# Kernel tuning notes

Measured on AMD Instinct MI355X. Metric: run time of the kernel, lower is better.

The kernel has to match this reference:

```python
import jax, jax.numpy as jnp
import numpy as np

DG = 8            # deformable_groups
MAX_RES = 10.0    # max_residual_magnitude
K = 9             # 3x3 kernel positions


def conv3(x, w, b):
    y = jax.lax.conv_general_dilated(x, w, (1, 1), [(1, 1), (1, 1)],
                                     dimension_numbers=('NCHW', 'OIHW', 'NCHW'))
    return y + b[None, :, None, None]


def lrelu(v):
    return jnp.where(v >= 0, v, 0.1 * v)


def deform_conv2d(x, offset, mask, weight, bias):
    # x: [B,C,H,W]; offset: [B,2*DG*K,H,W] (per group, K points, (y,x) interleaved)
    # mask: [B,DG*K,H,W]; weight: [O,C,3,3]; stride=1, pad=1, dil=1, groups=1
    B, C, H, W = x.shape
    Cg = C // DG
    off = offset.reshape(B, DG, K, 2, H, W)
    dtype = x.dtype
    dy = (jnp.arange(K) // 3 - 1).astype(dtype)
    dx = (jnp.arange(K) % 3 - 1).astype(dtype)
    py = off[:, :, :, 0] + jnp.arange(H, dtype=dtype)[None, None, None, :, None] + dy[None, None, :, None, None]
    px = off[:, :, :, 1] + jnp.arange(W, dtype=dtype)[None, None, None, None, :] + dx[None, None, :, None, None]
    y0 = jnp.floor(py)
    x0 = jnp.floor(px)
    x_flat = x.reshape(B, DG, Cg, H * W)
    m = mask.reshape(B, DG, K, H, W)
    acc = jnp.zeros((B, DG, Cg, K, H, W), dtype=dtype)
    for iy, wy in ((y0, y0 + 1.0 - py), (y0 + 1.0, py - y0)):
        for ix, wx in ((x0, x0 + 1.0 - px), (x0 + 1.0, px - x0)):
            valid = (iy >= 0) & (iy < H) & (ix >= 0) & (ix < W)
            yi = jnp.clip(iy, 0, H - 1).astype(jnp.int32)
            xi = jnp.clip(ix, 0, W - 1).astype(jnp.int32)
            idx = (yi * W + xi).reshape(B, DG, 1, K * H * W)
            g = jnp.take_along_axis(x_flat, idx, axis=3).reshape(B, DG, Cg, K, H, W)
            wgt = (wy * wx * valid.astype(dtype) * m)[:, :, None]  # mask folded in
            acc = acc + g * wgt
    O = weight.shape[0]
    out = jnp.einsum('bgckhw,ogck->bohw', acc, weight.reshape(O, DG, Cg, K))
    return out + bias[None, :, None, None]


def setup_inputs() -> dict:
    key = jax.random.key(0)
    ks = jax.random.split(key, 12)
    B, C, H, W = 4, 64, 128, 128
    inp = {
        'x': jax.random.normal(ks[0], (B, C, H, W), jnp.float32),
        'x_warped0': jax.random.normal(ks[1], (B, C, H, W), jnp.float32),
        'x_current': jax.random.normal(ks[2], (B, C, H, W), jnp.float32),
        'flow0': jax.random.normal(ks[3], (B, 2, H, W), jnp.float32),
        'w1': jax.random.normal(ks[4], (64, 130, 3, 3), jnp.float32) * 0.05,
        'b1': jnp.zeros((64,), jnp.float32),
        'w2': jax.random.normal(ks[5], (64, 64, 3, 3), jnp.float32) * 0.05,
        'b2': jnp.zeros((64,), jnp.float32),
        'w3': jax.random.normal(ks[6], (64, 64, 3, 3), jnp.float32) * 0.05,
        'b3': jnp.zeros((64,), jnp.float32),
        'w4': jax.random.normal(ks[7], (216, 64, 3, 3), jnp.float32) * 0.05,
        'b4': jnp.zeros((216,), jnp.float32),
        'weight': jax.random.normal(ks[8], (64, 64, 3, 3), jnp.float32) * 0.05,
        'bias': jnp.zeros((64,), jnp.float32),
    }
    return inp


def reference(x, x_warped0, x_current, flow0, w1, b1, w2, b2, w3, b3, w4, b4, weight, bias):
    # conv_offset stack on cat([x_warped0, x_current, flow0])
    feat = jnp.concatenate([x_warped0, x_current, flow0], axis=1)  # [B, 2C+2, H, W]
    o = lrelu(conv3(feat, w1, b1))
    o = lrelu(conv3(o, w2, b2))
    o = lrelu(conv3(o, w3, b3))
    o = conv3(o, w4, b4)  # [B, 3*K*DG, H, W]
    out1, out2, mask = jnp.split(o, 3, axis=1)
    offset = MAX_RES * jnp.tanh(jnp.concatenate([out1, out2], axis=1))  # [B, 2*K*DG, H, W]
    # flows[0].flip(1).repeat(1, K*DG, 1, 1): (y,x) flow tiled over all sample points
    offset = offset + jnp.tile(flow0[:, ::-1], (1, K * DG, 1, 1))
    mask = jax.nn.sigmoid(mask)
    return deform_conv2d(x, offset, mask, weight, bias)
```

## Files before the change

kernel.cpp:

```cpp
#include <hip/hip_runtime.h>
#include <math.h>

#define HH 128
#define WW 128
#define BB 4
#define HW (HH*WW)

typedef unsigned short u16;
typedef unsigned int u32;
typedef __bf16 bf16x8 __attribute__((ext_vector_type(8)));
typedef float f32x4 __attribute__((ext_vector_type(4)));

__device__ __forceinline__ u16 f2bf(float x) {
    u32 u = __float_as_uint(x);
    return (u16)((u + 0x7fffu + ((u >> 16) & 1u)) >> 16);
}
__device__ __forceinline__ float bf2f(u16 h) {
    return __uint_as_float(((u32)h) << 16);
}
__device__ __forceinline__ bf16x8 ld8(const u16* p) {
    union { uint4 u; bf16x8 v; } c;
    c.u = *(const uint4*)p;
    return c.v;
}
__device__ __forceinline__ bf16x8 cvt8(uint4 u) {
    union { uint4 u; bf16x8 v; } c;
    c.u = u;
    return c.v;
}

__global__ void split_w_k(const float* __restrict__ src, u16* __restrict__ dh,
                          u16* __restrict__ dl, int OC, int OCpad, int CIN, int CINpad)
{
    const int i = blockIdx.x * 256 + threadIdx.x;
    const int tot = OCpad * 9 * CINpad;
    if (i >= tot) return;
    const int oc = i / (9 * CINpad);
    const int r = i - oc * 9 * CINpad;
    const int tap = r / CINpad;
    const int cin = r - tap * CINpad;
    float v = 0.f;
    if (oc < OC && cin < CIN) v = src[((size_t)oc * CIN + cin) * 9 + tap];
    const u16 h = f2bf(v);
    dh[i] = h;
    dl[i] = f2bf(v - bf2f(h));
}

__global__ void pad_bias_k(const float* __restrict__ b, float* __restrict__ bp)
{
    const int i = blockIdx.x * 256 + threadIdx.x;
    if (i < 256) bp[i] = (i < 216) ? b[i] : 0.f;
}

__global__ void pack_dw_k(const float* __restrict__ wt, u16* __restrict__ Apack)
{
    const int i = blockIdx.x * 256 + threadIdx.x;
    if (i >= 36864) return;
    const int jj = i & 7;
    const int fr = (i >> 3) & 15;
    const int m  = (i >> 7) & 3;
    const int fq = (i >> 9) & 3;
    const int kk = i >> 11;
    const int oc = m * 16 + fr;
    const int j  = kk * 32 + fq * 8 + jj;
    const int tap = j >> 3, c = j & 7;
    const int g = tap / 9, kt = tap - g * 9;
    const int ch = g * 8 + c;
    Apack[i] = f2bf(wt[((size_t)oc * 64 + ch) * 9 + kt]);
}

template<int CREC>
__global__ __launch_bounds__(256) void pack_x_k(
    const float* __restrict__ A, const float* __restrict__ B2,
    const float* __restrict__ C3, u16* __restrict__ dst)
{
    const int i = blockIdx.x * 256 + threadIdx.x;
    const int b = i >> 14;
    const int px = i & 16383;
    u16* rec = dst + (size_t)i * (CREC * 2);

#pragma unroll
    for (int g = 0; g < CREC / 32; ++g) {
#pragma unroll
        for (int cb = 0; cb < 4; ++cb) {
            u32 hwv[4], lwv[4];
#pragma unroll
            for (int p = 0; p < 4; ++p) {
                float v[2];
#pragma unroll
                for (int e = 0; e < 2; ++e) {
                    const int c = g * 32 + cb * 8 + p * 2 + e;
                    float vv;
                    if (c < 64)       vv = A[((size_t)(b * 64 + c)) * HW + px];
                    else if (c < 128) vv = B2[((size_t)(b * 64 + c - 64)) * HW + px];
                    else if (c < 130) vv = C3[((size_t)(b * 2 + c - 128)) * HW + px];
                    else              vv = 0.f;
                    v[e] = vv;
                }
                const u16 h0 = f2bf(v[0]), h1 = f2bf(v[1]);
                const u16 l0 = f2bf(v[0] - bf2f(h0)), l1 = f2bf(v[1] - bf2f(h1));
                hwv[p] = (u32)h0 | ((u32)h1 << 16);
                lwv[p] = (u32)l0 | ((u32)l1 << 16);
            }
            uint4 H; H.x = hwv[0]; H.y = hwv[1]; H.z = hwv[2]; H.w = hwv[3];
            uint4 L; L.x = lwv[0]; L.y = lwv[1]; L.z = lwv[2]; L.w = lwv[3];
            *(uint4*)(rec + g * 64 + cb * 16)     = H;
            *(uint4*)(rec + g * 64 + cb * 16 + 8) = L;
        }
    }
}

template<int NCHUNK, int KGLAST, int MODE, bool RELU, bool PACKOUT, int MINW>
__global__ __launch_bounds__(256, MINW) void conv_pk_k(
    const u16* __restrict__ Xp, const u16* __restrict__ Wh, const u16* __restrict__ Wl,
    const float* __restrict__ bias, float* __restrict__ outf, u16* __restrict__ outp,
    int OCreal)
{
    const int ROWS = (MODE == 1) ? 8 : 4;
    const int NPX = (ROWS + 2) * 18;
    __shared__ u16 Xs[NPX * 136];
    const int CINpad = (NCHUNK - 1) * 64 + KGLAST * 32;
    const int CRECU16 = CINpad * 2;

    const int tile = blockIdx.x;
    const int h0 = (tile >> 3) * ROWS;
    const int w0 = (tile & 7) * 16;
    const int b = blockIdx.z;
    const int t = threadIdx.x;
    const int lane = t & 63, wv = t >> 6;
    const int fr = lane & 15, fq = lane >> 4;

    const int mg = wv >> 1, rg = wv & 1;
    const int mbase = (MODE == 1) ? (blockIdx.y * 8 + mg * 4) : 0;

    f32x4 acc0[4];
    f32x4 acc1[4][4];
    if (MODE == 0) {
        const float4 bv = *(const float4*)(bias + wv * 16 + 4 * fq);
#pragma unroll
        for (int n = 0; n < 4; ++n) {
            acc0[n][0] = bv.x; acc0[n][1] = bv.y; acc0[n][2] = bv.z; acc0[n][3] = bv.w;
        }
    } else {
#pragma unroll
        for (int m = 0; m < 4; ++m) {
            const float4 bv = *(const float4*)(bias + (mbase + m) * 16 + 4 * fq);
#pragma unroll
            for (int n = 0; n < 4; ++n) {
                acc1[m][n][0] = bv.x; acc1[m][n][1] = bv.y;
                acc1[m][n][2] = bv.z; acc1[m][n][3] = bv.w;
            }
        }
    }

    const u16* WhL = Wh + (size_t)fr * 9 * CINpad + 8 * fq;
    const u16* WlL = Wl + (size_t)fr * 9 * CINpad + 8 * fq;

#pragma unroll
    for (int chunk = 0; chunk < NCHUNK; ++chunk) {
        const int nkg = (chunk == NCHUNK - 1) ? KGLAST : 2;
        const int nu = nkg * 8;
        __syncthreads();
        for (int s = t; s < NPX * nu; s += 256) {
            const int px = s / nu, o = s - px * nu;
            const int hy = px / 18, hx = px - hy * 18;
            const int gy = h0 + hy - 1, gx = w0 + hx - 1;
            uint4 v; v.x = 0; v.y = 0; v.z = 0; v.w = 0;
            if (gy >= 0 && gy < HH && gx >= 0 && gx < WW)
                v = *(const uint4*)(Xp + ((size_t)(b * HW + gy * WW + gx)) * CRECU16
                                       + chunk * 128 + o * 8);
            *(uint4*)(Xs + px * 136 + o * 8) = v;
        }
        __syncthreads();

        if (MODE == 0) {
#pragma unroll
            for (int tap = 0; tap < 9; ++tap) {
                const int ky = tap / 3, kx = tap % 3;
#pragma unroll
                for (int kg = 0; kg < 2; ++kg) {
                    if (kg >= nkg) break;
                    const size_t off = (size_t)(wv * 144 + tap) * CINpad + chunk * 64 + kg * 32;
                    const bf16x8 Ah = ld8(WhL + off);
                    const bf16x8 Al = ld8(WlL + off);
#pragma unroll
                    for (int n = 0; n < 4; ++n) {
                        const int hp = (n + ky) * 18 + fr + kx;
                        const u16* Bp = Xs + hp * 136 + kg * 64 + fq * 16;
                        const bf16x8 Bh = ld8(Bp);
                        const bf16x8 Bl = ld8(Bp + 8);
                        acc0[n] = __builtin_amdgcn_mfma_f32_16x16x32_bf16(Ah, Bh, acc0[n], 0, 0, 0);
                        acc0[n] = __builtin_amdgcn_mfma_f32_16x16x32_bf16(Ah, Bl, acc0[n], 0, 0, 0);
                        acc0[n] = __builtin_amdgcn_mfma_f32_16x16x32_bf16(Al, Bh, acc0[n], 0, 0, 0);
                    }
                }
            }
        } else {
            auto PF = [&](int tap, bf16x8 (&Dh)[8], bf16x8 (&Dl)[8]) {
#pragma unroll
                for (int kg = 0; kg < 2; ++kg)
#pragma unroll
                    for (int m = 0; m < 4; ++m) {
                        const size_t off = (size_t)((mbase + m) * 144 + tap) * CINpad
                                         + chunk * 64 + kg * 32;
                        Dh[kg * 4 + m] = ld8(WhL + off);
                        Dl[kg * 4 + m] = ld8(WlL + off);
                    }
            };
            auto CMP = [&](int tap, bf16x8 (&Dh)[8], bf16x8 (&Dl)[8]) {
                const int ky = tap / 3, kx = tap - 3 * ky;
#pragma unroll
                for (int kg = 0; kg < 2; ++kg) {
#pragma unroll
                    for (int n = 0; n < 4; ++n) {
                        const int hp = (rg * 4 + n + ky) * 18 + fr + kx;
                        const u16* Bp = Xs + hp * 136 + kg * 64 + fq * 16;
                        const bf16x8 Bh = ld8(Bp);
                        const bf16x8 Bl = ld8(Bp + 8);
#pragma unroll
                        for (int m = 0; m < 4; ++m) {
                            acc1[m][n] = __builtin_amdgcn_mfma_f32_16x16x32_bf16(Dh[kg * 4 + m], Bh, acc1[m][n], 0, 0, 0);
                            acc1[m][n] = __builtin_amdgcn_mfma_f32_16x16x32_bf16(Dh[kg * 4 + m], Bl, acc1[m][n], 0, 0, 0);
                            acc1[m][n] = __builtin_amdgcn_mfma_f32_16x16x32_bf16(Dl[kg * 4 + m], Bh, acc1[m][n], 0, 0, 0);
                        }
                    }
                }
            };

            bf16x8 PaH[8], PaL[8], PbH[8], PbL[8];
            PF(0, PaH, PaL);
#pragma unroll 1
            for (int tp = 0; tp < 4; ++tp) {
                PF(2 * tp + 1, PbH, PbL);
                CMP(2 * tp, PaH, PaL);
                PF(2 * tp + 2, PaH, PaL);
                CMP(2 * tp + 1, PbH, PbL);
            }
            CMP(8, PaH, PaL);
        }
    }

    if (MODE == 1) {
#pragma unroll
        for (int m = 0; m < 4; ++m)
#pragma unroll
            for (int n = 0; n < 4; ++n)
#pragma unroll
                for (int i = 0; i < 4; ++i) {
                    const int oc = (mbase + m) * 16 + 4 * fq + i;
                    if (oc < OCreal) {
                        float v = acc1[m][n][i];
                        if (RELU) v = (v >= 0.f) ? v : 0.1f * v;
                        outf[((size_t)(b * OCreal + oc)) * HW + (h0 + rg * 4 + n) * WW + w0 + fr] = v;
                    }
                }
    } else if (!PACKOUT) {
#pragma unroll
        for (int n = 0; n < 4; ++n)
#pragma unroll
            for (int i = 0; i < 4; ++i) {
                const int oc = wv * 16 + 4 * fq + i;
                if (oc < OCreal) {
                    float v = acc0[n][i];
                    if (RELU) v = (v >= 0.f) ? v : 0.1f * v;
                    outf[((size_t)(b * OCreal + oc)) * HW + (h0 + n) * WW + w0 + fr] = v;
                }
            }
    } else {
        __syncthreads();
        const int coff = (wv >> 1) * 64 + (((wv << 1) + (fq >> 1)) & 3) * 16 + ((fq & 1) << 2);
#pragma unroll
        for (int n = 0; n < 4; ++n) {
            u16 hh[4], ll[4];
#pragma unroll
            for (int i = 0; i < 4; ++i) {
                float v = acc0[n][i];
                if (RELU) v = (v >= 0.f) ? v : 0.1f * v;
                hh[i] = f2bf(v);
                ll[i] = f2bf(v - bf2f(hh[i]));
            }
            uint2 H, L;
            H.x = (u32)hh[0] | ((u32)hh[1] << 16);
            H.y = (u32)hh[2] | ((u32)hh[3] << 16);
            L.x = (u32)ll[0] | ((u32)ll[1] << 16);
            L.y = (u32)ll[2] | ((u32)ll[3] << 16);
            const int pxe = n * 16 + fr;
            u16* E = Xs + pxe * 136 + coff;
            *(uint2*)E = H;
            *(uint2*)(E + 8) = L;
        }
        __syncthreads();
        for (int i = t; i < 1024; i += 256) {
            const int px = i >> 4, o = i & 15;
            const uint4 v = *(const uint4*)(Xs + px * 136 + o * 8);
            const int gp = (h0 + (px >> 4)) * WW + w0 + (px & 15);
            *(uint4*)(outp + ((size_t)(b * HW + gp)) * 128 + o * 8) = v;
        }
    }
}

__global__ __launch_bounds__(256) void transpose_xq_k(
    const float* __restrict__ x, float4* __restrict__ xq)
{
    const int i = blockIdx.x * 256 + threadIdx.x;
    const int pix = i & (HW - 1);
    const int q = (i >> 14) & 15;
    const int b = i >> 18;
    const float* xp = x + ((size_t)(b * 64 + q * 4)) * HW + pix;
    float4 v;
    v.x = xp[0]; v.y = xp[HW]; v.z = xp[2 * HW]; v.w = xp[3 * HW];
    xq[(size_t)(b * 16 + q) * HW + pix] = v;
}

__device__ __forceinline__ unsigned pk_bf16(float lo, float hi) {
    unsigned a = __float_as_uint(lo), b = __float_as_uint(hi);
    return ((a + 0x8000u) >> 16) | ((b + 0x8000u) & 0xffff0000u);
}

__global__ __launch_bounds__(256, 4) void deform_fused_k(
    const float4* __restrict__ xq, const float* __restrict__ o4,
    const float* __restrict__ flow, const uint4* __restrict__ Apack,
    const float* __restrict__ bias, float* __restrict__ out)
{
    __shared__ u16 sv[32 * 584];

    const int bid = blockIdx.x;
    const int b = bid >> 9;
    const int pix0 = (bid & 511) << 5;
    const int t = threadIdx.x;

    {
        const int gpx = t & 31, g = t >> 5;
        const int pix = pix0 + gpx;
        const int h = pix >> 7, w = pix & (WW - 1);
        const float fy = flow[((size_t)b * 2 + 1) * HW + pix];
        const float fx = flow[((size_t)b * 2 + 0) * HW + pix];
        const float* ob = o4 + (size_t)b * 216 * HW + pix;
        const float4* q0 = xq + (size_t)(b * 16 + g * 2) * HW;
        const float4* q1 = q0 + HW;

        int   code[9];
        float w00[9], w01[9], w10[9], w11[9];

#pragma unroll
        for (int k = 0; k < 9; ++k) {
            const float oy = ob[(size_t)(g * 18 + k * 2) * HW];
            const float ox = ob[(size_t)(g * 18 + k * 2 + 1) * HW];
            float mm = ob[(size_t)(144 + g * 9 + k) * HW];
            mm = __builtin_amdgcn_rcpf(1.f + __expf(-mm));

            const float ay = fabsf(oy), ax = fabsf(ox);
            const float ey = __expf(-2.f * ay), ex = __expf(-2.f * ax);
            float ty = (1.f - ey) * __builtin_amdgcn_rcpf(1.f + ey);
            float tx = (1.f - ex) * __builtin_amdgcn_rcpf(1.f + ex);
            ty = copysignf(ty, oy); tx = copysignf(tx, ox);

            const float ppy = 10.f * ty + fy + (float)(h + k / 3 - 1);
            const float ppx = 10.f * tx + fx + (float)(w + k % 3 - 1);

            const float y0f = floorf(ppy), x0f = floorf(ppx);
            const float ly = ppy - y0f, lx = ppx - x0f;
            const int iy0 = (int)y0f, ix0 = (int)x0f;
            const int iy1 = iy0 + 1,  ix1 = ix0 + 1;

            const float vy0 = (iy0 >= 0 && iy0 < HH) ? 1.f : 0.f;
            const float vy1 = (iy1 >= 0 && iy1 < HH) ? 1.f : 0.f;
            const float vx0 = (ix0 >= 0 && ix0 < WW) ? 1.f : 0.f;
            const float vx1 = (ix1 >= 0 && ix1 < WW) ? 1.f : 0.f;

            const int cy0 = min(max(iy0, 0), HH - 1);
            const int cy1 = min(max(iy1, 0), HH - 1);
            const int cx0 = min(max(ix0, 0), WW - 1);
            const int cx1 = min(max(ix1, 0), WW - 1);

            w00[k] = (1.f - ly) * (1.f - lx) * vy0 * vx0 * mm;
            w01[k] = (1.f - ly) * lx         * vy0 * vx1 * mm;
            w10[k] = ly         * (1.f - lx) * vy1 * vx0 * mm;
            w11[k] = ly         * lx         * vy1 * vx1 * mm;

            code[k] = (cy0 * WW + cx0) | ((cx1 - cx0) << 14) | ((cy1 - cy0) << 15);
        }

        u16* svp = sv + gpx * 584 + g * 72;
#pragma unroll
        for (int k = 0; k < 9; ++k) {
            const int i00 = code[k] & 16383;
            const int i01 = i00 + ((code[k] >> 14) & 1);
            const int i10 = i00 + (((code[k] >> 15) & 1) << 7);
            const int i11 = i10 + ((code[k] >> 14) & 1);

            const float4 a0 = q0[i00], a1 = q1[i00];
            const float4 b0 = q0[i01], b1 = q1[i01];
            const float4 c0 = q0[i10], c1 = q1[i10];
            const float4 d0 = q0[i11], d1 = q1[i11];
            const float W00 = w00[k], W01 = w01[k], W10 = w10[k], W11 = w11[k];

            float s0 = W00 * a0.x + W01 * b0.x + W10 * c0.x + W11 * d0.x;
            float s1 = W00 * a0.y + W01 * b0.y + W10 * c0.y + W11 * d0.y;
            float s2 = W00 * a0.z + W01 * b0.z + W10 * c0.z + W11 * d0.z;
            float s3 = W00 * a0.w + W01 * b0.w + W10 * c0.w + W11 * d0.w;
            float s4 = W00 * a1.x + W01 * b1.x + W10 * c1.x + W11 * d1.x;
            float s5 = W00 * a1.y + W01 * b1.y + W10 * c1.y + W11 * d1.y;
            float s6 = W00 * a1.z + W01 * b1.z + W10 * c1.z + W11 * d1.z;
            float s7 = W00 * a1.w + W01 * b1.w + W10 * c1.w + W11 * d1.w;

            uint4 P;
            P.x = pk_bf16(s0, s1);
            P.y = pk_bf16(s2, s3);
            P.z = pk_bf16(s4, s5);
            P.w = pk_bf16(s6, s7);
            *(uint4*)(svp + (size_t)k * 8) = P;
        }
    }
    __syncthreads();

    {
        const int lane = t & 63, wv = t >> 6;
        const int fr = lane & 15, fq = lane >> 4;

        f32x4 acc[2];
#pragma unroll
        for (int n = 0; n < 2; ++n) { acc[n][0] = 0.f; acc[n][1] = 0.f; acc[n][2] = 0.f; acc[n][3] = 0.f; }

#pragma unroll
        for (int kk = 0; kk < 18; ++kk) {
            const bf16x8 A = cvt8(Apack[((kk * 4 + fq) * 4 + wv) * 16 + fr]);
#pragma unroll
            for (int n = 0; n < 2; ++n) {
                const bf16x8 Bf = ld8(sv + (size_t)(n * 16 + fr) * 584 + kk * 32 + fq * 8);
                acc[n] = __builtin_amdgcn_mfma_f32_16x16x32_bf16(A, Bf, acc[n], 0, 0, 0);
            }
        }

        const float4 bv = *(const float4*)(bias + wv * 16 + 4 * fq);
        const float bb[4] = { bv.x, bv.y, bv.z, bv.w };
#pragma unroll
        for (int n = 0; n < 2; ++n) {
            const int pix = pix0 + n * 16 + fr;
#pragma unroll
            for (int i = 0; i < 4; ++i) {
                const int oc = wv * 16 + 4 * fq + i;
                out[((size_t)b * 64 + oc) * HW + pix] = acc[n][i] + bb[i];
            }
        }
    }
}

extern "C" void kernel_launch(void* const* d_in, const int* in_sizes, int n_in,
                              void* d_out, int out_size, void* d_ws, size_t ws_size,
                              hipStream_t stream)
{
    const float* x     = (const float*)d_in[0];
    const float* xw    = (const float*)d_in[1];
    const float* xc    = (const float*)d_in[2];
    const float* flow  = (const float*)d_in[3];
    const float* w1    = (const float*)d_in[4];
    const float* b1    = (const float*)d_in[5];
    const float* w2    = (const float*)d_in[6];
    const float* b2    = (const float*)d_in[7];
    const float* w3    = (const float*)d_in[8];
    const float* b3    = (const float*)d_in[9];
    const float* w4    = (const float*)d_in[10];
    const float* b4    = (const float*)d_in[11];
    const float* wt    = (const float*)d_in[12];
    const float* bias  = (const float*)d_in[13];
    float* out = (float*)d_out;

    char* ws = (char*)d_ws;
    u16*   X1p  = (u16*)(ws);
    float* o4   = (float*)(ws);
    u16*   buf1 = (u16*)(ws + 56623104);
    u16*   buf2 = (u16*)(ws + 73400320);
    u16* Apack = (u16*)(ws + 90177536);
    u16* W1h = (u16*)(ws + 90251264);
    u16* W1l = (u16*)(ws + 90435584);
    u16* W2h = (u16*)(ws + 90619904);
    u16* W2l = (u16*)(ws + 90693632);
    u16* W3h = (u16*)(ws + 90767360);
    u16* W3l = (u16*)(ws + 90841088);
    u16* W4h = (u16*)(ws + 90914816);
    u16* W4l = (u16*)(ws + 91209728);
    float* b4p = (float*)(ws + 91504640);

    const dim3 blk(256);

    split_w_k<<<dim3((64 * 9 * 160 + 255) / 256), blk, 0, stream>>>(w1, W1h, W1l, 64, 64, 130, 160);
    split_w_k<<<dim3((64 * 9 * 64 + 255) / 256), blk, 0, stream>>>(w2, W2h, W2l, 64, 64, 64, 64);
    split_w_k<<<dim3((64 * 9 * 64 + 255) / 256), blk, 0, stream>>>(w3, W3h, W3l, 64, 64, 64, 64);
    split_w_k<<<dim3((256 * 9 * 64 + 255) / 256), blk, 0, stream>>>(w4, W4h, W4l, 216, 256, 64, 64);
    pad_bias_k<<<dim3(1), blk, 0, stream>>>(b4, b4p);
    pack_dw_k<<<dim3(144), blk, 0, stream>>>(wt, Apack);

    pack_x_k<160><<<dim3(BB * HW / 256), blk, 0, stream>>>(xw, xc, flow, X1p);
    conv_pk_k<3, 1, 0, true, true, 2><<<dim3(256, 1, BB), blk, 0, stream>>>(
        X1p, W1h, W1l, b1, nullptr, buf1, 64);
    conv_pk_k<1, 2, 0, true, true, 2><<<dim3(256, 1, BB), blk, 0, stream>>>(
        buf1, W2h, W2l, b2, nullptr, buf2, 64);
    conv_pk_k<1, 2, 0, true, true, 2><<<dim3(256, 1, BB), blk, 0, stream>>>(
        buf2, W3h, W3l, b3, nullptr, buf1, 64);
    transpose_xq_k<<<dim3(BB * 16 * HW / 256), blk, 0, stream>>>(x, (float4*)buf2);
    conv_pk_k<1, 2, 1, false, false, 1><<<dim3(128, 2, BB), blk, 0, stream>>>(
        buf1, W4h, W4l, b4p, o4, nullptr, 216);

    deform_fused_k<<<dim3(BB * HW / 32), blk, 0, stream>>>(
        (const float4*)buf2, o4, flow, (const uint4*)Apack, bias, out);
}
```

Measured before the change: 332.0 us.

## Halve deform block pixel tile and split kernel points across two threads

The fused deformable kernel now handles 16 pixels per block instead of 32. Each pixel/group pair's 9 sampling points are split across two threads (4 and 5 points), which halves per-thread register arrays and the serial gather chain, doubles the grid, and halves shared memory per block. The cost is that each block now issues one MFMA per k-step instead of two, so the bf16 weight fragments loaded from global memory are reused across half as many pixels. The split is also uneven (4 vs 5 points), so some threads sit idle at the end.

```diff
diff --git a/kernel.cpp b/kernel.cpp
--- a/kernel.cpp
+++ b/kernel.cpp
@@ -322,16 +322,18 @@
     const float* __restrict__ flow, const uint4* __restrict__ Apack,
     const float* __restrict__ bias, float* __restrict__ out)
 {
-    __shared__ u16 sv[32 * 584];
+    __shared__ u16 sv[16 * 584];
 
     const int bid = blockIdx.x;
-    const int b = bid >> 9;
-    const int pix0 = (bid & 511) << 5;
+    const int b = bid >> 10;
+    const int pix0 = (bid & 1023) << 4;
     const int t = threadIdx.x;
 
     {
-        const int gpx = t & 31, g = t >> 5;
-        const int pix = pix0 + gpx;
+        const int px = t & 15, gk = t >> 4;
+        const int g = gk >> 1, kh = gk & 1;
+        const int kbase = kh * 4;
+        const int pix = pix0 + px;
         const int h = pix >> 7, w = pix & (WW - 1);
         const float fy = flow[((size_t)b * 2 + 1) * HW + pix];
         const float fx = flow[((size_t)b * 2 + 0) * HW + pix];
@@ -339,11 +341,13 @@
         const float4* q0 = xq + (size_t)(b * 16 + g * 2) * HW;
         const float4* q1 = q0 + HW;
 
-        int   code[9];
-        float w00[9], w01[9], w10[9], w11[9];
-
-#pragma unroll
-        for (int k = 0; k < 9; ++k) {
+        int   code[5];
+        float w00[5], w01[5], w10[5], w11[5];
+
+#pragma unroll
+        for (int j = 0; j < 5; ++j) {
+            if (j == 4 && !kh) break;
+            const int k = kbase + j;
             const float oy = ob[(size_t)(g * 18 + k * 2) * HW];
             const float ox = ob[(size_t)(g * 18 + k * 2 + 1) * HW];
             float mm = ob[(size_t)(144 + g * 9 + k) * HW];
@@ -373,27 +377,28 @@
             const int cx0 = min(max(ix0, 0), WW - 1);
             const int cx1 = min(max(ix1, 0), WW - 1);
 
-            w00[k] = (1.f - ly) * (1.f - lx) * vy0 * vx0 * mm;
-            w01[k] = (1.f - ly) * lx         * vy0 * vx1 * mm;
-            w10[k] = ly         * (1.f - lx) * vy1 * vx0 * mm;
-            w11[k] = ly         * lx         * vy1 * vx1 * mm;
-
-            code[k] = (cy0 * WW + cx0) | ((cx1 - cx0) << 14) | ((cy1 - cy0) << 15);
-        }
-
-        u16* svp = sv + gpx * 584 + g * 72;
-#pragma unroll
-        for (int k = 0; k < 9; ++k) {
-            const int i00 = code[k] & 16383;
-            const int i01 = i00 + ((code[k] >> 14) & 1);
-            const int i10 = i00 + (((code[k] >> 15) & 1) << 7);
-            const int i11 = i10 + ((code[k] >> 14) & 1);
+            w00[j] = (1.f - ly) * (1.f - lx) * vy0 * vx0 * mm;
+            w01[j] = (1.f - ly) * lx         * vy0 * vx1 * mm;
+            w10[j] = ly         * (1.f - lx) * vy1 * vx0 * mm;
+            w11[j] = ly         * lx         * vy1 * vx1 * mm;
+
+            code[j] = (cy0 * WW + cx0) | ((cx1 - cx0) << 14) | ((cy1 - cy0) << 15);
+        }
+
+        u16* svp = sv + px * 584 + g * 72 + kbase * 8;
+#pragma unroll
+        for (int j = 0; j < 5; ++j) {
+            if (j == 4 && !kh) break;
+            const int i00 = code[j] & 16383;
+            const int i01 = i00 + ((code[j] >> 14) & 1);
+            const int i10 = i00 + (((code[j] >> 15) & 1) << 7);
+            const int i11 = i10 + ((code[j] >> 14) & 1);
 
             const float4 a0 = q0[i00], a1 = q1[i00];
             const float4 b0 = q0[i01], b1 = q1[i01];
             const float4 c0 = q0[i10], c1 = q1[i10];
             const float4 d0 = q0[i11], d1 = q1[i11];
-            const float W00 = w00[k], W01 = w01[k], W10 = w10[k], W11 = w11[k];
+            const float W00 = w00[j], W01 = w01[j], W10 = w10[j], W11 = w11[j];
 
             float s0 = W00 * a0.x + W01 * b0.x + W10 * c0.x + W11 * d0.x;
             float s1 = W00 * a0.y + W01 * b0.y + W10 * c0.y + W11 * d0.y;
@@ -409,7 +414,7 @@
             P.y = pk_bf16(s2, s3);
             P.z = pk_bf16(s4, s5);
             P.w = pk_bf16(s6, s7);
-            *(uint4*)(svp + (size_t)k * 8) = P;
+            *(uint4*)(svp + (size_t)j * 8) = P;
         }
     }
     __syncthreads();
@@ -418,30 +423,22 @@
         const int lane = t & 63, wv = t >> 6;
         const int fr = lane & 15, fq = lane >> 4;
 
-        f32x4 acc[2];
-#pragma unroll
-        for (int n = 0; n < 2; ++n) { acc[n][0] = 0.f; acc[n][1] = 0.f; acc[n][2] = 0.f; acc[n][3] = 0.f; }
+        f32x4 acc;
+        acc[0] = 0.f; acc[1] = 0.f; acc[2] = 0.f; acc[3] = 0.f;
 
 #pragma unroll
         for (int kk = 0; kk < 18; ++kk) {
             const bf16x8 A = cvt8(Apack[((kk * 4 + fq) * 4 + wv) * 16 + fr]);
-#pragma unroll
-            for (int n = 0; n < 2; ++n) {
-                const bf16x8 Bf = ld8(sv + (size_t)(n * 16 + fr) * 584 + kk * 32 + fq * 8);
-                acc[n] = __builtin_amdgcn_mfma_f32_16x16x32_bf16(A, Bf, acc[n], 0, 0, 0);
-            }
+            const bf16x8 Bf = ld8(sv + (size_t)fr * 584 + kk * 32 + fq * 8);
+            acc = __builtin_amdgcn_mfma_f32_16x16x32_bf16(A, Bf, acc, 0, 0, 0);
         }
 
         const float4 bv = *(const float4*)(bias + wv * 16 + 4 * fq);
         const float bb[4] = { bv.x, bv.y, bv.z, bv.w };
 #pragma unroll
-        for (int n = 0; n < 2; ++n) {
-            const int pix = pix0 + n * 16 + fr;
-#pragma unroll
-            for (int i = 0; i < 4; ++i) {
-                const int oc = wv * 16 + 4 * fq + i;
-                out[((size_t)b * 64 + oc) * HW + pix] = acc[n][i] + bb[i];
-            }
+        for (int i = 0; i < 4; ++i) {
+            const int oc = wv * 16 + 4 * fq + i;
+            out[((size_t)b * 64 + oc) * HW + pix0 + fr] = acc[i] + bb[i];
         }
     }
 }
@@ -502,6 +499,6 @@
     conv_pk_k<1, 2, 1, false, false, 1><<<dim3(128, 2, BB), blk, 0, stream>>>(
         buf1, W4h, W4l, b4p, o4, nullptr, 216);
 
-    deform_fused_k<<<dim3(BB * HW / 32), blk, 0, stream>>>(
+    deform_fused_k<<<dim3(BB * HW / 16), blk, 0, stream>>>(
         (const float4*)buf2, o4, flow, (const uint4*)Apack, bias, out);
 }
```

Measured after the change: 343.6 us. 3.5% more time.
